# Optimization experiments

Hardware: AMD Instinct MI355X
Metric: run time of the kernel (lower is better)

## Reference

```python
import jax, jax.numpy as jnp
import numpy as np

EPS = 1e-5      # eps used in abs() and log()
BN_EPS = 1e-5   # torch BatchNorm2d default eps


def setup_inputs() -> dict:
    key = jax.random.key(0)
    ks = jax.random.split(key, 5)
    N, C, F, T = 16, 4, 257, 1000
    B, K = 8, 80
    xr = jax.random.normal(ks[0], (N, C, F, T), dtype=jnp.float32)
    xi = jax.random.normal(ks[1], (N, C, F, T), dtype=jnp.float32)
    # per-bin complex beamforming weights: (F, B, C) == Conv1d weight (B*F, 1, C) regrouped
    wr = jax.random.normal(ks[2], (F, B, C), dtype=jnp.float32) * 0.25
    wi = jax.random.normal(ks[3], (F, B, C), dtype=jnp.float32) * 0.25
    # nn.Linear(num_bins, spectra_filters, bias=False) weight: (K, F)
    w_proj = jax.random.normal(ks[4], (K, F), dtype=jnp.float32) * (1.0 / np.sqrt(F))
    gamma = jnp.ones((B,), dtype=jnp.float32)
    beta = jnp.zeros((B,), dtype=jnp.float32)
    return {"xr": xr, "xi": xi, "wr": wr, "wi": wi, "w_proj": w_proj,
            "gamma": gamma, "beta": beta}


def reference(xr, xi, wr, wi, w_proj, gamma, beta):
    # Grouped complex conv1d == per-bin complex beamform across mics:
    # out[n,b,t,f] = sum_c w[f,b,c] * x[n,c,f,t] (complex product)
    br = jnp.einsum('ncft,fbc->nbtf', xr, wr) - jnp.einsum('ncft,fbc->nbtf', xi, wi)
    bi = jnp.einsum('ncft,fbc->nbtf', xi, wr) + jnp.einsum('ncft,fbc->nbtf', xr, wi)
    mag = jnp.sqrt(br * br + bi * bi + EPS)              # (N, B, T, F)
    # Linear(F -> K), ReLU, log
    f = jax.nn.relu(jnp.einsum('nbtf,kf->nbtk', mag, w_proj))
    f = jnp.log(f + EPS)                                  # (N, B, T, K)
    # BatchNorm2d over channel axis B (training-mode batch statistics)
    mean = jnp.mean(f, axis=(0, 2, 3), keepdims=True)
    var = jnp.var(f, axis=(0, 2, 3), keepdims=True)
    f = (f - mean) * jax.lax.rsqrt(var + BN_EPS)
    f = f * gamma[None, :, None, None] + beta[None, :, None, None]
    N, B, T, K = f.shape
    # (N, B, T, K) -> (N, T, B*K)
    return jnp.transpose(f, (0, 2, 1, 3)).reshape(N, T, B * K)
```

## Files before the change

kernel.cpp:

```cpp
#include <hip/hip_runtime.h>
#include <math.h>

#define N_ 16
#define C_ 4
#define F_ 257
#define T_ 1000
#define B_ 8
#define K_ 80
#define BK_ 640
#define TT_ 32
#define NT_ 32
#define NBLK (N_ * NT_)
#define MSTR 260
#define WSTR 164
#define WTG  160

#define WT_OFF   0
#define PART_OFF (256 * 1024)
#define SS_OFF   (PART_OFF + NBLK * 16 * 8)

__global__ __launch_bounds__(160) void k_wt(const float* __restrict__ wp,
                                            float* __restrict__ wT) {
    int f = blockIdx.x;
    int s = threadIdx.x;
    int g = s / 20, r = s % 20;
    float v = 0.f;
    if (r < 10) v = wp[(g * 10 + r) * F_ + f];
    wT[f * WTG + s] = v;
}

__global__ __launch_bounds__(256, 2) void k_fused(
    const float* __restrict__ xr, const float* __restrict__ xi,
    const float* __restrict__ wr, const float* __restrict__ wi,
    const float* __restrict__ wT,
    float* __restrict__ out, double* __restrict__ partials) {

    const int tid = threadIdx.x;
    const int bid = blockIdx.x;
    const int tt = bid & (NT_ - 1);
    const int n  = bid >> 5;
    const int t0 = tt * TT_;

    __shared__ float magS[TT_][MSTR];
    __shared__ float wS[32][WSTR];
    __shared__ double redS[2][4][B_];

    const int kx = tid & 7;
    const int ty = tid >> 3;

    const int tb = t0 + kx * 4;
    const bool tload = (tb + 4 <= T_);

    float acc[B_][10];
#pragma unroll
    for (int b = 0; b < B_; ++b)
#pragma unroll
        for (int j = 0; j < 10; ++j) acc[b][j] = 0.f;

    const float* xrn = xr + (size_t)n * C_ * F_ * T_;
    const float* xin = xi + (size_t)n * C_ * F_ * T_;

    float4 pxr[C_], pxi[C_];
    if (tload) {
        const float* xrp = xrn + (size_t)ty * T_ + tb;
        const float* xip = xin + (size_t)ty * T_ + tb;
#pragma unroll
        for (int c = 0; c < C_; ++c) {
            pxr[c] = *(const float4*)(xrp + (size_t)c * F_ * T_);
            pxi[c] = *(const float4*)(xip + (size_t)c * F_ * T_);
        }
    }

    for (int ch = 0; ch < 8; ++ch) {
        const int f0 = ch * 32;
        const int f  = f0 + ty;

        __syncthreads();

#pragma unroll
        for (int r = 0; r < 5; ++r) {
            int off = kx * 4 + r * 32;
            *(float4*)&wS[ty][off] = *(const float4*)(wT + (size_t)f * WTG + off);
        }

        {
            float m[4][B_];
            if (tload) {
                float xrv[C_][4], xiv[C_][4];
#pragma unroll
                for (int c = 0; c < C_; ++c) {
                    xrv[c][0] = pxr[c].x; xrv[c][1] = pxr[c].y;
                    xrv[c][2] = pxr[c].z; xrv[c][3] = pxr[c].w;
                    xiv[c][0] = pxi[c].x; xiv[c][1] = pxi[c].y;
                    xiv[c][2] = pxi[c].z; xiv[c][3] = pxi[c].w;
                }
                const float* wrp = wr + (size_t)f * B_ * C_;
                const float* wip = wi + (size_t)f * B_ * C_;
#pragma unroll
                for (int b = 0; b < B_; ++b) {
                    float4 wrv = *(const float4*)(wrp + b * C_);
                    float4 wiv = *(const float4*)(wip + b * C_);
                    float wrc[4] = {wrv.x, wrv.y, wrv.z, wrv.w};
                    float wic[4] = {wiv.x, wiv.y, wiv.z, wiv.w};
#pragma unroll
                    for (int i = 0; i < 4; ++i) {
                        float br = 0.f, bi2 = 0.f;
#pragma unroll
                        for (int c = 0; c < C_; ++c) {
                            br  += xrv[c][i] * wrc[c] - xiv[c][i] * wic[c];
                            bi2 += xiv[c][i] * wrc[c] + xrv[c][i] * wic[c];
                        }
                        m[i][b] = sqrtf(br * br + bi2 * bi2 + 1e-5f);
                    }
                }
            } else {
#pragma unroll
                for (int i = 0; i < 4; ++i)
#pragma unroll
                    for (int b = 0; b < B_; ++b) m[i][b] = 0.f;
            }
#pragma unroll
            for (int i = 0; i < 4; ++i) {
                *(float4*)&magS[kx * 4 + i][ty * 8] =
                    make_float4(m[i][0], m[i][1], m[i][2], m[i][3]);
                *(float4*)&magS[kx * 4 + i][ty * 8 + 4] =
                    make_float4(m[i][4], m[i][5], m[i][6], m[i][7]);
            }
        }

        if (ch < 7 && tload) {
            const float* xrp = xrn + (size_t)(f0 + 32 + ty) * T_ + tb;
            const float* xip = xin + (size_t)(f0 + 32 + ty) * T_ + tb;
#pragma unroll
            for (int c = 0; c < C_; ++c) {
                pxr[c] = *(const float4*)(xrp + (size_t)c * F_ * T_);
                pxi[c] = *(const float4*)(xip + (size_t)c * F_ * T_);
            }
        }

        __syncthreads();

#pragma unroll 2
        for (int fc = 0; fc < 32; ++fc) {
            float4 m0 = *(const float4*)&magS[ty][fc * 8];
            float4 m1 = *(const float4*)&magS[ty][fc * 8 + 4];
            float4 w0 = *(const float4*)&wS[fc][kx * 20];
            float4 w1 = *(const float4*)&wS[fc][kx * 20 + 4];
            float2 w2 = *(const float2*)&wS[fc][kx * 20 + 8];
            float wj[10] = {w0.x, w0.y, w0.z, w0.w, w1.x, w1.y, w1.z, w1.w, w2.x, w2.y};
            float mb[B_] = {m0.x, m0.y, m0.z, m0.w, m1.x, m1.y, m1.z, m1.w};
#pragma unroll
            for (int b = 0; b < B_; ++b)
#pragma unroll
                for (int j = 0; j < 10; ++j)
                    acc[b][j] += mb[b] * wj[j];
        }
    }

    __syncthreads();
    if (tid < 160)
        wS[0][tid] = wT[(size_t)256 * WTG + tid];
    {
        int trow = tid >> 3;
        int b = tid & 7;
        int t = t0 + trow;
        float v = 0.f;
        if (t < T_) {
            const float* wrp = wr + (size_t)(256 * B_ + b) * C_;
            const float* wip = wi + (size_t)(256 * B_ + b) * C_;
            float br = 0.f, bi2 = 0.f;
#pragma unroll
            for (int c = 0; c < C_; ++c) {
                float xrv = xrn[((size_t)c * F_ + 256) * T_ + t];
                float xiv = xin[((size_t)c * F_ + 256) * T_ + t];
                br  += xrv * wrp[c] - xiv * wip[c];
                bi2 += xiv * wrp[c] + xrv * wip[c];
            }
            v = sqrtf(br * br + bi2 * bi2 + 1e-5f);
        }
        magS[trow][b] = v;
    }
    __syncthreads();
    {
        float4 m0 = *(const float4*)&magS[ty][0];
        float4 m1 = *(const float4*)&magS[ty][4];
        float4 w0 = *(const float4*)&wS[0][kx * 20];
        float4 w1 = *(const float4*)&wS[0][kx * 20 + 4];
        float2 w2 = *(const float2*)&wS[0][kx * 20 + 8];
        float wj[10] = {w0.x, w0.y, w0.z, w0.w, w1.x, w1.y, w1.z, w1.w, w2.x, w2.y};
        float mb[B_] = {m0.x, m0.y, m0.z, m0.w, m1.x, m1.y, m1.z, m1.w};
#pragma unroll
        for (int b = 0; b < B_; ++b)
#pragma unroll
            for (int j = 0; j < 10; ++j)
                acc[b][j] += mb[b] * wj[j];
    }

    float s1f[B_], s2f[B_];
#pragma unroll
    for (int b = 0; b < B_; ++b) { s1f[b] = 0.f; s2f[b] = 0.f; }
    const int t = t0 + ty;
    if (t < T_) {
        float* orow = out + ((size_t)n * T_ + t) * BK_ + kx * 10;
#pragma unroll
        for (int b = 0; b < B_; ++b) {
#pragma unroll
            for (int j = 0; j < 10; ++j) {
                float v = fmaxf(acc[b][j], 0.0f);
                v = __logf(v + 1e-5f);
                orow[b * K_ + j] = v;
                s1f[b] += v;
                s2f[b] += v * v;
            }
        }
    }
    const int wid = tid >> 6, lane = tid & 63;
#pragma unroll
    for (int b = 0; b < B_; ++b) {
        double d1 = (double)s1f[b], d2 = (double)s2f[b];
#pragma unroll
        for (int off = 32; off; off >>= 1) {
            d1 += __shfl_down(d1, off);
            d2 += __shfl_down(d2, off);
        }
        if (lane == 0) { redS[0][wid][b] = d1; redS[1][wid][b] = d2; }
    }
    __syncthreads();
    if (tid < 8) {
        partials[(size_t)bid * 16 + tid] =
            redS[0][0][tid] + redS[0][1][tid] + redS[0][2][tid] + redS[0][3][tid];
    } else if (tid >= 64 && tid < 72) {
        int b = tid - 64;
        partials[(size_t)bid * 16 + 8 + b] =
            redS[1][0][b] + redS[1][1][b] + redS[1][2][b] + redS[1][3][b];
    }
}

__global__ __launch_bounds__(256) void k_bnstats(
    const double* __restrict__ partials,
    const float* __restrict__ gamma, const float* __restrict__ beta,
    float* __restrict__ ss) {
    const int b = threadIdx.x >> 5;
    const int i = threadIdx.x & 31;
    double s1 = 0.0, s2 = 0.0;
    for (int j = i; j < NBLK; j += 32) {
        s1 += partials[(size_t)j * 16 + b];
        s2 += partials[(size_t)j * 16 + 8 + b];
    }
#pragma unroll
    for (int off = 16; off; off >>= 1) {
        s1 += __shfl_down(s1, off);
        s2 += __shfl_down(s2, off);
    }
    if (i == 0) {
        const double cnt = (double)N_ * T_ * K_;
        double mean = s1 / cnt;
        double var = s2 / cnt - mean * mean;
        float scale = gamma[b] * (float)(1.0 / sqrt(var + 1e-5));
        float shift = beta[b] - (float)mean * scale;
        ss[b] = scale;
        ss[B_ + b] = shift;
    }
}

__global__ __launch_bounds__(256) void k_bnapply(float* __restrict__ out,
                                                 const float* __restrict__ ss) {
    size_t i4 = (size_t)blockIdx.x * 256 + threadIdx.x;
    int k4 = (int)(i4 % (BK_ / 4));
    int b = k4 / (K_ / 4);
    float scale = ss[b], shift = ss[B_ + b];
    float4* p = (float4*)out + i4;
    float4 v = *p;
    v.x = v.x * scale + shift;
    v.y = v.y * scale + shift;
    v.z = v.z * scale + shift;
    v.w = v.w * scale + shift;
    *p = v;
}

extern "C" void kernel_launch(void* const* d_in, const int* in_sizes, int n_in,
                              void* d_out, int out_size, void* d_ws, size_t ws_size,
                              hipStream_t stream) {
    const float* xr = (const float*)d_in[0];
    const float* xi = (const float*)d_in[1];
    const float* wr = (const float*)d_in[2];
    const float* wi = (const float*)d_in[3];
    const float* w_proj = (const float*)d_in[4];
    const float* gamma = (const float*)d_in[5];
    const float* beta = (const float*)d_in[6];
    float* out = (float*)d_out;

    float* wT = (float*)((char*)d_ws + WT_OFF);
    double* partials = (double*)((char*)d_ws + PART_OFF);
    float* ss = (float*)((char*)d_ws + SS_OFF);

    k_wt<<<F_, 160, 0, stream>>>(w_proj, wT);
    k_fused<<<NBLK, 256, 0, stream>>>(xr, xi, wr, wi, wT, out, partials);
    k_bnstats<<<1, 256, 0, stream>>>(partials, gamma, beta, ss);
    k_bnapply<<<10000, 256, 0, stream>>>(out, ss);
}
```

Baseline: 149.6 us.

## Remap projection GEMM threads so weights are wavefront-uniform scalar loads

The thread mapping of the F->K projection is reorganised so each wavefront owns a 20-wide slice of K (kg read via readfirstlane), letting weight reads come straight from global memory as uniform scalar loads instead of being staged through an LDS weight tile. Each thread now covers one time step and four beam channels instead of eight beams by ten outputs, and output rows are written with float4 stores. The weight transpose kernel drops its padding, and the BN partial-sum reduction is changed to match the new layout. This removes LDS traffic and a staging loop, at the cost of relying on scalar-cache hits for the weight reads and a different register and bank-access pattern.

```diff
diff --git a/kernel.cpp b/kernel.cpp
--- a/kernel.cpp
+++ b/kernel.cpp
@@ -12,21 +12,17 @@
 #define NT_ 32
 #define NBLK (N_ * NT_)
 #define MSTR 260
-#define WSTR 164
-#define WTG  160
+#define WKS  80
 
 #define WT_OFF   0
-#define PART_OFF (256 * 1024)
+#define PART_OFF (128 * 1024)
 #define SS_OFF   (PART_OFF + NBLK * 16 * 8)
 
-__global__ __launch_bounds__(160) void k_wt(const float* __restrict__ wp,
-                                            float* __restrict__ wT) {
+__global__ __launch_bounds__(80) void k_wt(const float* __restrict__ wp,
+                                           float* __restrict__ wT) {
     int f = blockIdx.x;
-    int s = threadIdx.x;
-    int g = s / 20, r = s % 20;
-    float v = 0.f;
-    if (r < 10) v = wp[(g * 10 + r) * F_ + f];
-    wT[f * WTG + s] = v;
+    int k = threadIdx.x;
+    wT[f * WKS + k] = wp[k * F_ + f];
 }
 
 __global__ __launch_bounds__(256, 2) void k_fused(
@@ -42,28 +38,31 @@
     const int t0 = tt * TT_;
 
     __shared__ float magS[TT_][MSTR];
-    __shared__ float wS[32][WSTR];
-    __shared__ double redS[2][4][B_];
-
-    const int kx = tid & 7;
-    const int ty = tid >> 3;
-
-    const int tb = t0 + kx * 4;
+    __shared__ double redS1[4][2][4];
+    __shared__ double redS2[4][2][4];
+
+    const int t_loc = tid & 31;
+    const int bh    = (tid >> 5) & 1;
+    const int kg    = __builtin_amdgcn_readfirstlane(tid >> 6);
+
+    const int sfr = tid >> 3;
+    const int stq = tid & 7;
+    const int tb  = t0 + stq * 4;
     const bool tload = (tb + 4 <= T_);
 
-    float acc[B_][10];
-#pragma unroll
-    for (int b = 0; b < B_; ++b)
-#pragma unroll
-        for (int j = 0; j < 10; ++j) acc[b][j] = 0.f;
+    float acc[4][20];
+#pragma unroll
+    for (int jb = 0; jb < 4; ++jb)
+#pragma unroll
+        for (int j = 0; j < 20; ++j) acc[jb][j] = 0.f;
 
     const float* xrn = xr + (size_t)n * C_ * F_ * T_;
     const float* xin = xi + (size_t)n * C_ * F_ * T_;
 
     float4 pxr[C_], pxi[C_];
     if (tload) {
-        const float* xrp = xrn + (size_t)ty * T_ + tb;
-        const float* xip = xin + (size_t)ty * T_ + tb;
+        const float* xrp = xrn + (size_t)sfr * T_ + tb;
+        const float* xip = xin + (size_t)sfr * T_ + tb;
 #pragma unroll
         for (int c = 0; c < C_; ++c) {
             pxr[c] = *(const float4*)(xrp + (size_t)c * F_ * T_);
@@ -73,15 +72,9 @@
 
     for (int ch = 0; ch < 8; ++ch) {
         const int f0 = ch * 32;
-        const int f  = f0 + ty;
+        const int f  = f0 + sfr;
 
         __syncthreads();
-
-#pragma unroll
-        for (int r = 0; r < 5; ++r) {
-            int off = kx * 4 + r * 32;
-            *(float4*)&wS[ty][off] = *(const float4*)(wT + (size_t)f * WTG + off);
-        }
 
         {
             float m[4][B_];
@@ -121,16 +114,16 @@
             }
 #pragma unroll
             for (int i = 0; i < 4; ++i) {
-                *(float4*)&magS[kx * 4 + i][ty * 8] =
+                *(float4*)&magS[stq * 4 + i][sfr * 8] =
                     make_float4(m[i][0], m[i][1], m[i][2], m[i][3]);
-                *(float4*)&magS[kx * 4 + i][ty * 8 + 4] =
+                *(float4*)&magS[stq * 4 + i][sfr * 8 + 4] =
                     make_float4(m[i][4], m[i][5], m[i][6], m[i][7]);
             }
         }
 
         if (ch < 7 && tload) {
-            const float* xrp = xrn + (size_t)(f0 + 32 + ty) * T_ + tb;
-            const float* xip = xin + (size_t)(f0 + 32 + ty) * T_ + tb;
+            const float* xrp = xrn + (size_t)(f0 + 32 + sfr) * T_ + tb;
+            const float* xip = xin + (size_t)(f0 + 32 + sfr) * T_ + tb;
 #pragma unroll
             for (int c = 0; c < C_; ++c) {
                 pxr[c] = *(const float4*)(xrp + (size_t)c * F_ * T_);
@@ -140,26 +133,23 @@
 
         __syncthreads();
 
+        const float* wchunk = wT + (size_t)f0 * WKS + kg * 20;
 #pragma unroll 2
         for (int fc = 0; fc < 32; ++fc) {
-            float4 m0 = *(const float4*)&magS[ty][fc * 8];
-            float4 m1 = *(const float4*)&magS[ty][fc * 8 + 4];
-            float4 w0 = *(const float4*)&wS[fc][kx * 20];
-            float4 w1 = *(const float4*)&wS[fc][kx * 20 + 4];
-            float2 w2 = *(const float2*)&wS[fc][kx * 20 + 8];
-            float wj[10] = {w0.x, w0.y, w0.z, w0.w, w1.x, w1.y, w1.z, w1.w, w2.x, w2.y};
-            float mb[B_] = {m0.x, m0.y, m0.z, m0.w, m1.x, m1.y, m1.z, m1.w};
-#pragma unroll
-            for (int b = 0; b < B_; ++b)
-#pragma unroll
-                for (int j = 0; j < 10; ++j)
-                    acc[b][j] += mb[b] * wj[j];
+            float4 mv = *(const float4*)&magS[t_loc][fc * 8 + bh * 4];
+            float wv[20];
+#pragma unroll
+            for (int j = 0; j < 20; ++j) wv[j] = wchunk[fc * WKS + j];
+            float mbv[4] = {mv.x, mv.y, mv.z, mv.w};
+#pragma unroll
+            for (int jb = 0; jb < 4; ++jb)
+#pragma unroll
+                for (int j = 0; j < 20; ++j)
+                    acc[jb][j] += mbv[jb] * wv[j];
         }
     }
 
     __syncthreads();
-    if (tid < 160)
-        wS[0][tid] = wT[(size_t)256 * WTG + tid];
     {
         int trow = tid >> 3;
         int b = tid & 7;
@@ -182,57 +172,61 @@
     }
     __syncthreads();
     {
-        float4 m0 = *(const float4*)&magS[ty][0];
-        float4 m1 = *(const float4*)&magS[ty][4];
-        float4 w0 = *(const float4*)&wS[0][kx * 20];
-        float4 w1 = *(const float4*)&wS[0][kx * 20 + 4];
-        float2 w2 = *(const float2*)&wS[0][kx * 20 + 8];
-        float wj[10] = {w0.x, w0.y, w0.z, w0.w, w1.x, w1.y, w1.z, w1.w, w2.x, w2.y};
-        float mb[B_] = {m0.x, m0.y, m0.z, m0.w, m1.x, m1.y, m1.z, m1.w};
-#pragma unroll
-        for (int b = 0; b < B_; ++b)
-#pragma unroll
-            for (int j = 0; j < 10; ++j)
-                acc[b][j] += mb[b] * wj[j];
-    }
-
-    float s1f[B_], s2f[B_];
-#pragma unroll
-    for (int b = 0; b < B_; ++b) { s1f[b] = 0.f; s2f[b] = 0.f; }
-    const int t = t0 + ty;
+        float4 mv = *(const float4*)&magS[t_loc][bh * 4];
+        const float* wtail = wT + (size_t)256 * WKS + kg * 20;
+        float mbv[4] = {mv.x, mv.y, mv.z, mv.w};
+#pragma unroll
+        for (int jb = 0; jb < 4; ++jb)
+#pragma unroll
+            for (int j = 0; j < 20; ++j)
+                acc[jb][j] += mbv[jb] * wtail[j];
+    }
+
+    float s1f[4], s2f[4];
+#pragma unroll
+    for (int jb = 0; jb < 4; ++jb) { s1f[jb] = 0.f; s2f[jb] = 0.f; }
+    const int t = t0 + t_loc;
     if (t < T_) {
-        float* orow = out + ((size_t)n * T_ + t) * BK_ + kx * 10;
-#pragma unroll
-        for (int b = 0; b < B_; ++b) {
-#pragma unroll
-            for (int j = 0; j < 10; ++j) {
-                float v = fmaxf(acc[b][j], 0.0f);
+        float* obase = out + ((size_t)n * T_ + t) * BK_ + (bh * 4) * K_ + kg * 20;
+#pragma unroll
+        for (int jb = 0; jb < 4; ++jb) {
+            float vv[20];
+#pragma unroll
+            for (int j = 0; j < 20; ++j) {
+                float v = fmaxf(acc[jb][j], 0.0f);
                 v = __logf(v + 1e-5f);
-                orow[b * K_ + j] = v;
-                s1f[b] += v;
-                s2f[b] += v * v;
-            }
-        }
-    }
-    const int wid = tid >> 6, lane = tid & 63;
-#pragma unroll
-    for (int b = 0; b < B_; ++b) {
-        double d1 = (double)s1f[b], d2 = (double)s2f[b];
-#pragma unroll
-        for (int off = 32; off; off >>= 1) {
-            d1 += __shfl_down(d1, off);
-            d2 += __shfl_down(d2, off);
-        }
-        if (lane == 0) { redS[0][wid][b] = d1; redS[1][wid][b] = d2; }
+                vv[j] = v;
+                s1f[jb] += v;
+                s2f[jb] += v * v;
+            }
+            float* orow = obase + jb * K_;
+#pragma unroll
+            for (int q = 0; q < 5; ++q)
+                *(float4*)(orow + q * 4) =
+                    make_float4(vv[q * 4], vv[q * 4 + 1], vv[q * 4 + 2], vv[q * 4 + 3]);
+        }
+    }
+    const int wav = tid >> 6;
+#pragma unroll
+    for (int jb = 0; jb < 4; ++jb) {
+        double d1 = (double)s1f[jb], d2 = (double)s2f[jb];
+#pragma unroll
+        for (int off = 16; off; off >>= 1) {
+            d1 += __shfl_xor(d1, off);
+            d2 += __shfl_xor(d2, off);
+        }
+        if ((tid & 31) == 0) { redS1[wav][bh][jb] = d1; redS2[wav][bh][jb] = d2; }
     }
     __syncthreads();
     if (tid < 8) {
+        int bh2 = tid >> 2, jb2 = tid & 3;
         partials[(size_t)bid * 16 + tid] =
-            redS[0][0][tid] + redS[0][1][tid] + redS[0][2][tid] + redS[0][3][tid];
+            redS1[0][bh2][jb2] + redS1[1][bh2][jb2] + redS1[2][bh2][jb2] + redS1[3][bh2][jb2];
     } else if (tid >= 64 && tid < 72) {
-        int b = tid - 64;
-        partials[(size_t)bid * 16 + 8 + b] =
-            redS[1][0][b] + redS[1][1][b] + redS[1][2][b] + redS[1][3][b];
+        int id = tid - 64;
+        int bh2 = id >> 2, jb2 = id & 3;
+        partials[(size_t)bid * 16 + 8 + id] =
+            redS2[0][bh2][jb2] + redS2[1][bh2][jb2] + redS2[2][bh2][jb2] + redS2[3][bh2][jb2];
     }
 }
 
@@ -294,7 +288,7 @@
     double* partials = (double*)((char*)d_ws + PART_OFF);
     float* ss = (float*)((char*)d_ws + SS_OFF);
 
-    k_wt<<<F_, 160, 0, stream>>>(w_proj, wT);
+    k_wt<<<F_, 80, 0, stream>>>(w_proj, wT);
     k_fused<<<NBLK, 256, 0, stream>>>(xr, xi, wr, wi, wT, out, partials);
     k_bnstats<<<1, 256, 0, stream>>>(partials, gamma, beta, ss);
     k_bnapply<<<10000, 256, 0, stream>>>(out, ss);
```

Result: slower. 157.8 us (+5.5%).
